# Optimization experiments

Measured on AMD Instinct MI355X. Metric: run time of the kernel, lower is better.

The kernel has to match this reference:

```python
import jax, jax.numpy as jnp
import numpy as np

LAYER_SIZES = [256, 256, 256]
SPLIT_HALF = True
B, F0, D = 512, 32, 32


def setup_inputs() -> dict:
    key = jax.random.key(0)
    ks = jax.random.split(key, 7)
    field_nums = [F0]
    for i, s in enumerate(LAYER_SIZES):
        field_nums.append(s // 2 if (SPLIT_HALF and i != len(LAYER_SIZES) - 1) else (s // 2 if SPLIT_HALF else s))
    # field_nums = [32, 128, 128, 128] (last entry unused for weights)
    inp = {
        'feat': jax.random.normal(ks[0], (B, F0, D), dtype=jnp.float32),
        'W0': jax.random.normal(ks[1], (LAYER_SIZES[0], field_nums[0], F0), dtype=jnp.float32) * 0.05,
        'b0': jnp.zeros((LAYER_SIZES[0],), dtype=jnp.float32),
        'W1': jax.random.normal(ks[2], (LAYER_SIZES[1], field_nums[1], F0), dtype=jnp.float32) * 0.05,
        'b1': jnp.zeros((LAYER_SIZES[1],), dtype=jnp.float32),
        'W2': jax.random.normal(ks[3], (LAYER_SIZES[2], field_nums[2], F0), dtype=jnp.float32) * 0.05,
        'b2': jnp.zeros((LAYER_SIZES[2],), dtype=jnp.float32),
    }
    return inp


def _cin_layer(h, feat, W, b):
    # h: [B,H,D], feat: [B,F0,D], W: [K,H,F0], b: [K] -> out [B,K,D]
    # outer product per embedding dim, then 1x1 conv (full [H,F0] contraction)
    z = jnp.einsum('bid,bjd->bdij', h, feat)          # [B,D,H,F0]
    out = jnp.einsum('bdij,kij->bkd', z, W) + b[None, :, None]
    return jax.nn.relu(out)


def reference(feat, W0, b0, W1, b1, W2, b2):
    Ws = [W0, W1, W2]
    bs = [b0, b1, b2]
    h = feat
    p = []
    n_layers = len(LAYER_SIZES)
    for l, K in enumerate(LAYER_SIZES):
        out = _cin_layer(h, feat, Ws[l], bs[l])        # [B,K,D]
        if SPLIT_HALF and l != n_layers - 1:
            h = out[:, :K // 2, :]
            direct = out[:, K // 2:, :]
        else:
            direct = out
            h = out
        p.append(direct)
    return jnp.concatenate(p, axis=1).sum(-1)          # [B, sum of direct sizes]
```

## Files before the change

### kernel.cpp

```cpp
#include <hip/hip_runtime.h>
#include <hip/hip_fp16.h>
#include <stdint.h>


typedef _Float16 half8_t __attribute__((ext_vector_type(8)));
typedef float f32x4 __attribute__((ext_vector_type(4)));
typedef uint32_t u32x4 __attribute__((ext_vector_type(4)));

union H8 {
  half8_t h;
  uint32_t u[4];
  u32x4 q;
};

#define AS1 __attribute__((address_space(1)))
#define AS3 __attribute__((address_space(3)))

static __device__ __forceinline__ uint32_t pkmul(uint32_t x, uint32_t y) {
  __half2 a = __builtin_bit_cast(__half2, x);
  __half2 b = __builtin_bit_cast(__half2, y);
  __half2 r = __hmul2(a, b);
  return __builtin_bit_cast(uint32_t, r);
}

static __device__ __forceinline__ uint32_t pack2h(float a, float b) {
  __half2 r = __floats2half2_rn(a, b);
  return __builtin_bit_cast(uint32_t, r);
}

__global__ void prep_kernel(const float* __restrict__ W0, const float* __restrict__ W1,
                            const float* __restrict__ W2, const float* __restrict__ feat,
                            uint16_t* __restrict__ Wt0, uint16_t* __restrict__ Wt1,
                            uint16_t* __restrict__ Wt2,
                            uint16_t* __restrict__ F16, uint16_t* __restrict__ hW0) {
  int blk = blockIdx.x;
  if (blk < 1152) {
    const float* W; uint16_t* Wt; int FLsh, base;
    if (blk < 128)      { W = W0; Wt = Wt0; FLsh = 5; base = 0; }
    else if (blk < 640) { W = W1; Wt = Wt1; FLsh = 7; base = 128; }
    else                { W = W2; Wt = Wt2; FLsh = 7; base = 640; }
    int idx4 = (blk - base) * 256 + threadIdx.x;
    int jg = idx4 & 3;
    int i = (idx4 >> 2) & ((1 << FLsh) - 1);
    int k = idx4 >> (2 + FLsh);
    const float* src = W + ((size_t)(k << FLsh) + i) * 32 + jg * 8;
    float4 x0 = *(const float4*)(src);
    float4 x1 = *(const float4*)(src + 4);
    u32x4 o;
    o[0] = pack2h(x0.x, x0.y);
    o[1] = pack2h(x0.z, x0.w);
    o[2] = pack2h(x1.x, x1.y);
    o[3] = pack2h(x1.z, x1.w);
    int q = i >> 2, il = i & 3, kq = k >> 6, kl = k & 63;
    int slot = jg ^ ((kl >> 1) & 3);
    size_t byteoff = (size_t)(q * 4 + kq) * 16384 + il * 4096 + kl * 64 + (slot << 4);
    *(u32x4*)((char*)Wt + byteoff) = o;
  } else {
    int m = (blk - 1152) * 256 + threadIdx.x;
    int b = m >> 5, d = m & 31;
    const float* fb = feat + (size_t)b * 1024 + d;
    uint16_t hs[32];
#pragma unroll
    for (int j = 0; j < 32; ++j)
      hs[j] = __half_as_ushort(__float2half(fb[j * 32]));
    int mgrp = m >> 7, l15 = m & 15, mt = (m >> 4) & 7;
#pragma unroll
    for (int j = 0; j < 32; ++j)
      hW0[((size_t)j * 128 + mgrp) * 128 + l15 * 8 + mt] = hs[j];
#pragma unroll
    for (int c = 0; c < 4; ++c) {
      u32x4 qv;
      qv[0] = (uint32_t)hs[c * 8 + 0] | ((uint32_t)hs[c * 8 + 1] << 16);
      qv[1] = (uint32_t)hs[c * 8 + 2] | ((uint32_t)hs[c * 8 + 3] << 16);
      qv[2] = (uint32_t)hs[c * 8 + 4] | ((uint32_t)hs[c * 8 + 5] << 16);
      qv[3] = (uint32_t)hs[c * 8 + 6] | ((uint32_t)hs[c * 8 + 7] << 16);
      *(u32x4*)(F16 + (size_t)m * 32 + c * 8) = qv;
    }
  }
}

template <int FL>
__global__ __launch_bounds__(256, 2) void gemm_cin(
    const uint16_t* __restrict__ hW,
    const uint16_t* __restrict__ wt,
    const uint16_t* __restrict__ f16m,
    const float* __restrict__ bias,
    uint16_t* __restrict__ hWn,
    float* __restrict__ outp,
    int obase, int klo) {
  constexpr int NCHK = FL / 4;
  constexpr int NCM = NCHK - 1;
  __shared__ __align__(16) char smem[34816];
  const int tid = threadIdx.x;
  const int lane = tid & 63, w = tid >> 6;
  const int l15 = lane & 15, lq = lane >> 4;
  const int kq = blockIdx.x & 3, mgrp = blockIdx.x >> 2;
  const int m0g = mgrp * 128, k0g = kq * 64;

  H8 ff[8];
#pragma unroll
  for (int mt = 0; mt < 8; ++mt)
    ff[mt].q = *(const u32x4*)(f16m + (size_t)(m0g + mt * 16 + l15) * 32 + lq * 8);

  const char* wsrc = (const char*)wt + kq * 16384 + tid * 16;
  char* wdst = smem + tid * 16;
  const char* hsrc = (const char*)hW + (size_t)mgrp * 256 + (tid & 15) * 16 +
                     (size_t)(tid >> 4) * 32768;
  char* hdst = smem + 32768 + (tid >> 4) * 256 + (tid & 15) * 16;

#define STAGE(QQ, PAR)                                                        \
  { size_t qo_ = (size_t)((QQ) & NCM);                                        \
    const char* s_ = wsrc + qo_ * 65536;                                      \
    char* d_ = wdst + (PAR) * 16384;                                          \
    _Pragma("unroll") for (int c_ = 0; c_ < 4; ++c_)                          \
      __builtin_amdgcn_global_load_lds((const AS1 uint32_t*)(s_ + c_ * 4096), \
                                       (AS3 uint32_t*)(d_ + c_ * 4096), 16, 0, 0); \
    if (tid < 64)                                                             \
      __builtin_amdgcn_global_load_lds(                                       \
          (const AS1 uint32_t*)(hsrc + qo_ * 131072),                         \
          (AS3 uint32_t*)(hdst + (PAR) * 1024), 16, 0, 0); }

  const char* arb = smem + (w * 16 + l15) * 64 + ((lq ^ ((l15 >> 1) & 3)) << 4);
  const char* hrb = smem + 32768 + l15 * 16;

  f32x4 acc[8];
#pragma unroll
  for (int mt = 0; mt < 8; ++mt) acc[mt] = (f32x4){0.f, 0.f, 0.f, 0.f};

  STAGE(0, 0)
  asm volatile("s_waitcnt vmcnt(0)" ::: "memory");
  __builtin_amdgcn_s_barrier();

#define ISTEP(AI, HI)                                                              \
  { H8 b0_, b1_, b2_, b3_, b4_, b5_, b6_, b7_;                                     \
    uint32_t hd_;                                                                  \
    hd_ = __builtin_amdgcn_perm(HI.u[0], HI.u[0], 0x01000100u);                    \
    _Pragma("unroll") for (int c_ = 0; c_ < 4; ++c_) b0_.u[c_] = pkmul(ff[0].u[c_], hd_); \
    hd_ = __builtin_amdgcn_perm(HI.u[0], HI.u[0], 0x03020302u);                    \
    _Pragma("unroll") for (int c_ = 0; c_ < 4; ++c_) b1_.u[c_] = pkmul(ff[1].u[c_], hd_); \
    hd_ = __builtin_amdgcn_perm(HI.u[1], HI.u[1], 0x01000100u);                    \
    _Pragma("unroll") for (int c_ = 0; c_ < 4; ++c_) b2_.u[c_] = pkmul(ff[2].u[c_], hd_); \
    hd_ = __builtin_amdgcn_perm(HI.u[1], HI.u[1], 0x03020302u);                    \
    _Pragma("unroll") for (int c_ = 0; c_ < 4; ++c_) b3_.u[c_] = pkmul(ff[3].u[c_], hd_); \
    hd_ = __builtin_amdgcn_perm(HI.u[2], HI.u[2], 0x01000100u);                    \
    _Pragma("unroll") for (int c_ = 0; c_ < 4; ++c_) b4_.u[c_] = pkmul(ff[4].u[c_], hd_); \
    hd_ = __builtin_amdgcn_perm(HI.u[2], HI.u[2], 0x03020302u);                    \
    _Pragma("unroll") for (int c_ = 0; c_ < 4; ++c_) b5_.u[c_] = pkmul(ff[5].u[c_], hd_); \
    hd_ = __builtin_amdgcn_perm(HI.u[3], HI.u[3], 0x01000100u);                    \
    _Pragma("unroll") for (int c_ = 0; c_ < 4; ++c_) b6_.u[c_] = pkmul(ff[6].u[c_], hd_); \
    hd_ = __builtin_amdgcn_perm(HI.u[3], HI.u[3], 0x03020302u);                    \
    _Pragma("unroll") for (int c_ = 0; c_ < 4; ++c_) b7_.u[c_] = pkmul(ff[7].u[c_], hd_); \
    __builtin_amdgcn_s_setprio(1);                                                 \
    acc[0] = __builtin_amdgcn_mfma_f32_16x16x32_f16(AI.h, b0_.h, acc[0], 0, 0, 0); \
    acc[1] = __builtin_amdgcn_mfma_f32_16x16x32_f16(AI.h, b1_.h, acc[1], 0, 0, 0); \
    acc[2] = __builtin_amdgcn_mfma_f32_16x16x32_f16(AI.h, b2_.h, acc[2], 0, 0, 0); \
    acc[3] = __builtin_amdgcn_mfma_f32_16x16x32_f16(AI.h, b3_.h, acc[3], 0, 0, 0); \
    acc[4] = __builtin_amdgcn_mfma_f32_16x16x32_f16(AI.h, b4_.h, acc[4], 0, 0, 0); \
    acc[5] = __builtin_amdgcn_mfma_f32_16x16x32_f16(AI.h, b5_.h, acc[5], 0, 0, 0); \
    acc[6] = __builtin_amdgcn_mfma_f32_16x16x32_f16(AI.h, b6_.h, acc[6], 0, 0, 0); \
    acc[7] = __builtin_amdgcn_mfma_f32_16x16x32_f16(AI.h, b7_.h, acc[7], 0, 0, 0); \
    __builtin_amdgcn_s_setprio(0); }

#pragma unroll 1
  for (int q = 0; q < NCHK; ++q) {
    const int par = q & 1;
    const char* ab = arb + par * 16384;
    const char* hb = hrb + par * 1024;
    H8 a0, a1, a2, a3, h0, h1, h2, h3;
    a0.q = *(const u32x4*)(ab);
    a1.q = *(const u32x4*)(ab + 4096);
    a2.q = *(const u32x4*)(ab + 8192);
    a3.q = *(const u32x4*)(ab + 12288);
    h0.q = *(const u32x4*)(hb);
    h1.q = *(const u32x4*)(hb + 256);
    h2.q = *(const u32x4*)(hb + 512);
    h3.q = *(const u32x4*)(hb + 768);
    STAGE(q + 1, par ^ 1)
    ISTEP(a0, h0)
    ISTEP(a1, h1)
    ISTEP(a2, h2)
    ISTEP(a3, h3)
    asm volatile("s_waitcnt vmcnt(0)" ::: "memory");
    __builtin_amdgcn_s_barrier();
  }
#undef ISTEP
#undef STAGE

  f32x4 bv = *(const f32x4*)(bias + k0g + w * 16 + lq * 4);
  float v[8][4];
#pragma unroll
  for (int mt = 0; mt < 8; ++mt)
#pragma unroll
    for (int r = 0; r < 4; ++r) {
      float x = acc[mt][r] + bv[r];
      v[mt][r] = x > 0.f ? x : 0.f;
    }

  if (hWn != nullptr && kq < 2) {
#pragma unroll
    for (int mt = 0; mt < 8; ++mt)
#pragma unroll
      for (int r = 0; r < 4; ++r) {
        int k = k0g + w * 16 + lq * 4 + r;
        hWn[((size_t)k * 128 + mgrp) * 128 + l15 * 8 + mt] =
            __half_as_ushort(__float2half(v[mt][r]));
      }
  }

#pragma unroll
  for (int p = 0; p < 4; ++p) {
    f32x4 sv;
#pragma unroll
    for (int r = 0; r < 4; ++r) {
      float x = v[2 * p][r] + v[2 * p + 1][r];
      x += __shfl_xor(x, 1);
      x += __shfl_xor(x, 2);
      x += __shfl_xor(x, 4);
      x += __shfl_xor(x, 8);
      sv[r] = x;
    }
    if (l15 == 0 && k0g >= klo) {
      float* ob = outp + (size_t)(mgrp * 4 + p) * 512 + obase + k0g + w * 16 +
                  lq * 4 - klo;
      *(f32x4*)ob = sv;
    }
  }
}

extern "C" void kernel_launch(void* const* d_in, const int* in_sizes, int n_in,
                              void* d_out, int out_size, void* d_ws, size_t ws_size,
                              hipStream_t stream) {
  const float* feat = (const float*)d_in[0];
  const float* W0 = (const float*)d_in[1];
  const float* b0 = (const float*)d_in[2];
  const float* W1 = (const float*)d_in[3];
  const float* b1 = (const float*)d_in[4];
  const float* W2 = (const float*)d_in[5];
  const float* b2 = (const float*)d_in[6];
  float* out = (float*)d_out;
  char* ws = (char*)d_ws;

  uint16_t* Wt0 = (uint16_t*)(ws + 0x000000);
  uint16_t* Wt1 = (uint16_t*)(ws + 0x080000);
  uint16_t* Wt2 = (uint16_t*)(ws + 0x280000);
  uint16_t* F16 = (uint16_t*)(ws + 0x480000);
  uint16_t* hW0 = (uint16_t*)(ws + 0x580000);
  uint16_t* hW1 = (uint16_t*)(ws + 0x680000);
  uint16_t* hW2 = (uint16_t*)(ws + 0xA80000);

  prep_kernel<<<1216, 256, 0, stream>>>(W0, W1, W2, feat, Wt0, Wt1, Wt2, F16, hW0);

  gemm_cin<32><<<512, 256, 0, stream>>>(hW0, Wt0, F16, b0, hW1, out, 0, 128);
  gemm_cin<128><<<512, 256, 0, stream>>>(hW1, Wt1, F16, b1, hW2, out, 128, 128);
  gemm_cin<128><<<512, 256, 0, stream>>>(hW2, Wt2, F16, b2, (uint16_t*)nullptr,
                                         out, 256, 0);
}
```

Measured before the change: 103.4 us.

## Restructure CIN GEMM: 512-thread blocks, per-wave M tiles, pre-duplicated h layout

Reworks the CIN GEMM so each of 8 waves owns a 16-row M tile and all 64 K outputs, instead of 4 waves each owning 16 K and 128 M. The h values are stored pre-duplicated as half2 words in a per-row layout. They are loaded straight into registers from global memory, which removes the LDS staging and the perm instructions. Weights are staged in larger double-buffered chunks of 8 i-values with 64KB+ of shared memory. Output reduction now goes through shared memory across wave pairs. The trade-off is that each lane does a weight LDS read per MFMA, the h scratch buffers double in size, and larger blocks may lower occupancy.

```diff
diff --git a/kernel.cpp b/kernel.cpp
--- a/kernel.cpp
+++ b/kernel.cpp
@@ -23,6 +23,10 @@
   return __builtin_bit_cast(uint32_t, r);
 }
 
+static __device__ __forceinline__ uint32_t dup2h(float a) {
+  return (uint32_t)__half_as_ushort(__float2half(a)) * 0x10001u;
+}
+
 static __device__ __forceinline__ uint32_t pack2h(float a, float b) {
   __half2 r = __floats2half2_rn(a, b);
   return __builtin_bit_cast(uint32_t, r);
@@ -32,7 +36,7 @@
                             const float* __restrict__ W2, const float* __restrict__ feat,
                             uint16_t* __restrict__ Wt0, uint16_t* __restrict__ Wt1,
                             uint16_t* __restrict__ Wt2,
-                            uint16_t* __restrict__ F16, uint16_t* __restrict__ hW0) {
+                            uint16_t* __restrict__ F16, uint32_t* __restrict__ hd0) {
   int blk = blockIdx.x;
   if (blk < 1152) {
     const float* W; uint16_t* Wt; int FLsh, base;
@@ -63,10 +67,11 @@
 #pragma unroll
     for (int j = 0; j < 32; ++j)
       hs[j] = __half_as_ushort(__float2half(fb[j * 32]));
-    int mgrp = m >> 7, l15 = m & 15, mt = (m >> 4) & 7;
-#pragma unroll
-    for (int j = 0; j < 32; ++j)
-      hW0[((size_t)j * 128 + mgrp) * 128 + l15 * 8 + mt] = hs[j];
+    int mb16 = m >> 4, l15 = m & 15;
+#pragma unroll
+    for (int i = 0; i < 32; ++i)
+      hd0[((size_t)(mb16 * 8 + (i >> 2)) * 16 + l15) * 4 + (i & 3)] =
+          (uint32_t)hs[i] * 0x10001u;
 #pragma unroll
     for (int c = 0; c < 4; ++c) {
       u32x4 qv;
@@ -80,150 +85,144 @@
 }
 
 template <int FL>
-__global__ __launch_bounds__(256, 2) void gemm_cin(
-    const uint16_t* __restrict__ hW,
+__global__ __launch_bounds__(512, 4) void gemm_cin(
+    const uint32_t* __restrict__ hdup,
     const uint16_t* __restrict__ wt,
     const uint16_t* __restrict__ f16m,
     const float* __restrict__ bias,
-    uint16_t* __restrict__ hWn,
+    uint32_t* __restrict__ hdn,
     float* __restrict__ outp,
     int obase, int klo) {
-  constexpr int NCHK = FL / 4;
+  constexpr int NCHK = FL / 8;
   constexpr int NCM = NCHK - 1;
-  __shared__ __align__(16) char smem[34816];
+  __shared__ __align__(16) char smem[67584];
   const int tid = threadIdx.x;
   const int lane = tid & 63, w = tid >> 6;
   const int l15 = lane & 15, lq = lane >> 4;
   const int kq = blockIdx.x & 3, mgrp = blockIdx.x >> 2;
-  const int m0g = mgrp * 128, k0g = kq * 64;
-
-  H8 ff[8];
-#pragma unroll
-  for (int mt = 0; mt < 8; ++mt)
-    ff[mt].q = *(const u32x4*)(f16m + (size_t)(m0g + mt * 16 + l15) * 32 + lq * 8);
-
-  const char* wsrc = (const char*)wt + kq * 16384 + tid * 16;
-  char* wdst = smem + tid * 16;
-  const char* hsrc = (const char*)hW + (size_t)mgrp * 256 + (tid & 15) * 16 +
-                     (size_t)(tid >> 4) * 32768;
-  char* hdst = smem + 32768 + (tid >> 4) * 256 + (tid & 15) * 16;
-
-#define STAGE(QQ, PAR)                                                        \
-  { size_t qo_ = (size_t)((QQ) & NCM);                                        \
-    const char* s_ = wsrc + qo_ * 65536;                                      \
-    char* d_ = wdst + (PAR) * 16384;                                          \
-    _Pragma("unroll") for (int c_ = 0; c_ < 4; ++c_)                          \
-      __builtin_amdgcn_global_load_lds((const AS1 uint32_t*)(s_ + c_ * 4096), \
-                                       (AS3 uint32_t*)(d_ + c_ * 4096), 16, 0, 0); \
-    if (tid < 64)                                                             \
-      __builtin_amdgcn_global_load_lds(                                       \
-          (const AS1 uint32_t*)(hsrc + qo_ * 131072),                         \
-          (AS3 uint32_t*)(hdst + (PAR) * 1024), 16, 0, 0); }
-
-  const char* arb = smem + (w * 16 + l15) * 64 + ((lq ^ ((l15 >> 1) & 3)) << 4);
-  const char* hrb = smem + 32768 + l15 * 16;
-
-  f32x4 acc[8];
-#pragma unroll
-  for (int mt = 0; mt < 8; ++mt) acc[mt] = (f32x4){0.f, 0.f, 0.f, 0.f};
+  const int mb16 = mgrp * 8 + w;
+
+  H8 ff;
+  ff.q = *(const u32x4*)(f16m + (size_t)(mb16 * 16 + l15) * 32 + lq * 8);
+
+  const char* wbase = (const char*)wt + kq * 16384;
+
+#define STAGE(CN, PAR)                                                        \
+  { _Pragma("unroll") for (int im_ = 0; im_ < 2; ++im_) {                     \
+      const char* s_ = wbase + (size_t)((2 * (CN) + im_) * 4) * 16384 + tid * 16; \
+      char* d_ = smem + (PAR) * 32768 + im_ * 16384 + tid * 16;               \
+      __builtin_amdgcn_global_load_lds((const AS1 uint32_t*)(s_),             \
+                                       (AS3 uint32_t*)(d_), 16, 0, 0);        \
+      __builtin_amdgcn_global_load_lds((const AS1 uint32_t*)(s_ + 8192),      \
+                                       (AS3 uint32_t*)(d_ + 8192), 16, 0, 0); \
+    } }
+
+  const char* hsrc = (const char*)hdup + (size_t)mb16 * (FL / 4) * 256 + l15 * 16;
+
+#define HLD(CN, D0, D1)                                                       \
+  { const char* p_ = hsrc + (size_t)(2 * (CN)) * 256;                         \
+    D0 = *(const u32x4*)(p_);                                                 \
+    D1 = *(const u32x4*)(p_ + 256); }
+
+  u32x4 hc0, hc1, hn0, hn1;
 
   STAGE(0, 0)
+  HLD(0, hc0, hc1)
+
+  f32x4 acc0 = {0.f, 0.f, 0.f, 0.f}, acc1 = acc0, acc2 = acc0, acc3 = acc0;
+  const char* rlane = smem + l15 * 64 + ((lq ^ ((l15 >> 1) & 3)) << 4);
+
   asm volatile("s_waitcnt vmcnt(0)" ::: "memory");
   __builtin_amdgcn_s_barrier();
 
-#define ISTEP(AI, HI)                                                              \
-  { H8 b0_, b1_, b2_, b3_, b4_, b5_, b6_, b7_;                                     \
-    uint32_t hd_;                                                                  \
-    hd_ = __builtin_amdgcn_perm(HI.u[0], HI.u[0], 0x01000100u);                    \
-    _Pragma("unroll") for (int c_ = 0; c_ < 4; ++c_) b0_.u[c_] = pkmul(ff[0].u[c_], hd_); \
-    hd_ = __builtin_amdgcn_perm(HI.u[0], HI.u[0], 0x03020302u);                    \
-    _Pragma("unroll") for (int c_ = 0; c_ < 4; ++c_) b1_.u[c_] = pkmul(ff[1].u[c_], hd_); \
-    hd_ = __builtin_amdgcn_perm(HI.u[1], HI.u[1], 0x01000100u);                    \
-    _Pragma("unroll") for (int c_ = 0; c_ < 4; ++c_) b2_.u[c_] = pkmul(ff[2].u[c_], hd_); \
-    hd_ = __builtin_amdgcn_perm(HI.u[1], HI.u[1], 0x03020302u);                    \
-    _Pragma("unroll") for (int c_ = 0; c_ < 4; ++c_) b3_.u[c_] = pkmul(ff[3].u[c_], hd_); \
-    hd_ = __builtin_amdgcn_perm(HI.u[2], HI.u[2], 0x01000100u);                    \
-    _Pragma("unroll") for (int c_ = 0; c_ < 4; ++c_) b4_.u[c_] = pkmul(ff[4].u[c_], hd_); \
-    hd_ = __builtin_amdgcn_perm(HI.u[2], HI.u[2], 0x03020302u);                    \
-    _Pragma("unroll") for (int c_ = 0; c_ < 4; ++c_) b5_.u[c_] = pkmul(ff[5].u[c_], hd_); \
-    hd_ = __builtin_amdgcn_perm(HI.u[3], HI.u[3], 0x01000100u);                    \
-    _Pragma("unroll") for (int c_ = 0; c_ < 4; ++c_) b6_.u[c_] = pkmul(ff[6].u[c_], hd_); \
-    hd_ = __builtin_amdgcn_perm(HI.u[3], HI.u[3], 0x03020302u);                    \
-    _Pragma("unroll") for (int c_ = 0; c_ < 4; ++c_) b7_.u[c_] = pkmul(ff[7].u[c_], hd_); \
-    __builtin_amdgcn_s_setprio(1);                                                 \
-    acc[0] = __builtin_amdgcn_mfma_f32_16x16x32_f16(AI.h, b0_.h, acc[0], 0, 0, 0); \
-    acc[1] = __builtin_amdgcn_mfma_f32_16x16x32_f16(AI.h, b1_.h, acc[1], 0, 0, 0); \
-    acc[2] = __builtin_amdgcn_mfma_f32_16x16x32_f16(AI.h, b2_.h, acc[2], 0, 0, 0); \
-    acc[3] = __builtin_amdgcn_mfma_f32_16x16x32_f16(AI.h, b3_.h, acc[3], 0, 0, 0); \
-    acc[4] = __builtin_amdgcn_mfma_f32_16x16x32_f16(AI.h, b4_.h, acc[4], 0, 0, 0); \
-    acc[5] = __builtin_amdgcn_mfma_f32_16x16x32_f16(AI.h, b5_.h, acc[5], 0, 0, 0); \
-    acc[6] = __builtin_amdgcn_mfma_f32_16x16x32_f16(AI.h, b6_.h, acc[6], 0, 0, 0); \
-    acc[7] = __builtin_amdgcn_mfma_f32_16x16x32_f16(AI.h, b7_.h, acc[7], 0, 0, 0); \
-    __builtin_amdgcn_s_setprio(0); }
+#define ISTEP(PAR, G, II, HV)                                                      \
+  { const char* rb_ = rlane + (PAR) * 32768 + (G) * 16384 + (II) * 4096;           \
+    H8 w0_, w1_, w2_, w3_, b_;                                                     \
+    w0_.q = *(const u32x4*)(rb_);                                                  \
+    w1_.q = *(const u32x4*)(rb_ + 1024);                                           \
+    w2_.q = *(const u32x4*)(rb_ + 2048);                                           \
+    w3_.q = *(const u32x4*)(rb_ + 3072);                                           \
+    uint32_t hv_ = (HV);                                                           \
+    H8 b2_;                                                                        \
+    _Pragma("unroll") for (int c_ = 0; c_ < 4; ++c_) b2_.u[c_] = pkmul(ff.u[c_], hv_); \
+    b_ = b2_;                                                                      \
+    acc0 = __builtin_amdgcn_mfma_f32_16x16x32_f16(w0_.h, b_.h, acc0, 0, 0, 0);     \
+    acc1 = __builtin_amdgcn_mfma_f32_16x16x32_f16(w1_.h, b_.h, acc1, 0, 0, 0);     \
+    acc2 = __builtin_amdgcn_mfma_f32_16x16x32_f16(w2_.h, b_.h, acc2, 0, 0, 0);     \
+    acc3 = __builtin_amdgcn_mfma_f32_16x16x32_f16(w3_.h, b_.h, acc3, 0, 0, 0); }
 
 #pragma unroll 1
-  for (int q = 0; q < NCHK; ++q) {
-    const int par = q & 1;
-    const char* ab = arb + par * 16384;
-    const char* hb = hrb + par * 1024;
-    H8 a0, a1, a2, a3, h0, h1, h2, h3;
-    a0.q = *(const u32x4*)(ab);
-    a1.q = *(const u32x4*)(ab + 4096);
-    a2.q = *(const u32x4*)(ab + 8192);
-    a3.q = *(const u32x4*)(ab + 12288);
-    h0.q = *(const u32x4*)(hb);
-    h1.q = *(const u32x4*)(hb + 256);
-    h2.q = *(const u32x4*)(hb + 512);
-    h3.q = *(const u32x4*)(hb + 768);
-    STAGE(q + 1, par ^ 1)
-    ISTEP(a0, h0)
-    ISTEP(a1, h1)
-    ISTEP(a2, h2)
-    ISTEP(a3, h3)
+  for (int c = 0; c < NCHK; ++c) {
+    const int par = c & 1;
+    STAGE((c + 1) & NCM, par ^ 1)
+    HLD((c + 1) & NCM, hn0, hn1)
+    ISTEP(par, 0, 0, hc0[0])
+    ISTEP(par, 0, 1, hc0[1])
+    ISTEP(par, 0, 2, hc0[2])
+    ISTEP(par, 0, 3, hc0[3])
+    ISTEP(par, 1, 0, hc1[0])
+    ISTEP(par, 1, 1, hc1[1])
+    ISTEP(par, 1, 2, hc1[2])
+    ISTEP(par, 1, 3, hc1[3])
+    hc0 = hn0;
+    hc1 = hn1;
     asm volatile("s_waitcnt vmcnt(0)" ::: "memory");
     __builtin_amdgcn_s_barrier();
   }
 #undef ISTEP
 #undef STAGE
-
-  f32x4 bv = *(const f32x4*)(bias + k0g + w * 16 + lq * 4);
-  float v[8][4];
-#pragma unroll
-  for (int mt = 0; mt < 8; ++mt)
+#undef HLD
+
+  float v[4][4];
+  {
+    f32x4 aq[4] = {acc0, acc1, acc2, acc3};
+#pragma unroll
+    for (int kt = 0; kt < 4; ++kt) {
+      f32x4 bv = *(const f32x4*)(bias + kq * 64 + kt * 16 + lq * 4);
+#pragma unroll
+      for (int r = 0; r < 4; ++r) {
+        float x = aq[kt][r] + bv[r];
+        v[kt][r] = x > 0.f ? x : 0.f;
+      }
+    }
+  }
+
+  if (hdn != nullptr && kq < 2) {
+#pragma unroll
+    for (int kt = 0; kt < 4; ++kt) {
+      int i4 = kq * 16 + kt * 4 + lq;
+      u32x4 du;
+#pragma unroll
+      for (int r = 0; r < 4; ++r) du[r] = dup2h(v[kt][r]);
+      *(u32x4*)((char*)hdn + ((size_t)(mb16 * 32 + i4) * 16 + l15) * 16) = du;
+    }
+  }
+
+  float* psum = (float*)(smem + 65536);
+#pragma unroll
+  for (int kt = 0; kt < 4; ++kt)
 #pragma unroll
     for (int r = 0; r < 4; ++r) {
-      float x = acc[mt][r] + bv[r];
-      v[mt][r] = x > 0.f ? x : 0.f;
-    }
-
-  if (hWn != nullptr && kq < 2) {
-#pragma unroll
-    for (int mt = 0; mt < 8; ++mt)
-#pragma unroll
-      for (int r = 0; r < 4; ++r) {
-        int k = k0g + w * 16 + lq * 4 + r;
-        hWn[((size_t)k * 128 + mgrp) * 128 + l15 * 8 + mt] =
-            __half_as_ushort(__float2half(v[mt][r]));
-      }
-  }
-
-#pragma unroll
-  for (int p = 0; p < 4; ++p) {
-    f32x4 sv;
-#pragma unroll
-    for (int r = 0; r < 4; ++r) {
-      float x = v[2 * p][r] + v[2 * p + 1][r];
+      float x = v[kt][r];
       x += __shfl_xor(x, 1);
       x += __shfl_xor(x, 2);
       x += __shfl_xor(x, 4);
       x += __shfl_xor(x, 8);
-      sv[r] = x;
-    }
-    if (l15 == 0 && k0g >= klo) {
-      float* ob = outp + (size_t)(mgrp * 4 + p) * 512 + obase + k0g + w * 16 +
-                  lq * 4 - klo;
-      *(f32x4*)ob = sv;
-    }
+      v[kt][r] = x;
+    }
+  if (l15 == 0) {
+#pragma unroll
+    for (int kt = 0; kt < 4; ++kt)
+#pragma unroll
+      for (int r = 0; r < 4; ++r)
+        psum[w * 64 + kt * 16 + lq * 4 + r] = v[kt][r];
+  }
+  __builtin_amdgcn_s_barrier();
+  if ((w & 1) == 0) {
+    int b = mgrp * 4 + (w >> 1);
+    float s = psum[w * 64 + lane] + psum[(w + 1) * 64 + lane];
+    int k = kq * 64 + lane;
+    if (k >= klo) outp[(size_t)b * 512 + obase + k - klo] = s;
   }
 }
 
@@ -244,14 +243,14 @@
   uint16_t* Wt1 = (uint16_t*)(ws + 0x080000);
   uint16_t* Wt2 = (uint16_t*)(ws + 0x280000);
   uint16_t* F16 = (uint16_t*)(ws + 0x480000);
-  uint16_t* hW0 = (uint16_t*)(ws + 0x580000);
-  uint16_t* hW1 = (uint16_t*)(ws + 0x680000);
-  uint16_t* hW2 = (uint16_t*)(ws + 0xA80000);
-
-  prep_kernel<<<1216, 256, 0, stream>>>(W0, W1, W2, feat, Wt0, Wt1, Wt2, F16, hW0);
-
-  gemm_cin<32><<<512, 256, 0, stream>>>(hW0, Wt0, F16, b0, hW1, out, 0, 128);
-  gemm_cin<128><<<512, 256, 0, stream>>>(hW1, Wt1, F16, b1, hW2, out, 128, 128);
-  gemm_cin<128><<<512, 256, 0, stream>>>(hW2, Wt2, F16, b2, (uint16_t*)nullptr,
+  uint32_t* hd0 = (uint32_t*)(ws + 0x580000);
+  uint32_t* hd1 = (uint32_t*)(ws + 0x780000);
+  uint32_t* hd2 = (uint32_t*)(ws + 0xF80000);
+
+  prep_kernel<<<1216, 256, 0, stream>>>(W0, W1, W2, feat, Wt0, Wt1, Wt2, F16, hd0);
+
+  gemm_cin<32><<<512, 512, 0, stream>>>(hd0, Wt0, F16, b0, hd1, out, 0, 128);
+  gemm_cin<128><<<512, 512, 0, stream>>>(hd1, Wt1, F16, b1, hd2, out, 128, 128);
+  gemm_cin<128><<<512, 512, 0, stream>>>(hd2, Wt2, F16, b2, (uint32_t*)nullptr,
                                          out, 256, 0);
 }
```

Result: faster. 98.39 us (-4.9%).
